# Kernel tuning notes

Measured on AMD Instinct MI355X. Metric: run time of the kernel, lower is better.

The kernel has to match this reference:

```python
import jax, jax.numpy as jnp
import numpy as np

B, T, E, H, VIN, VOUT = 64, 64, 64, 128, 256, 32000


def setup_inputs() -> dict:
    key = jax.random.key(0)
    ks = jax.random.split(key, 14)
    s = 0.08  # ~1/sqrt(hidden), torch-style init scale, avoids gate saturation
    return {
        "src": jax.random.randint(ks[0], (B, T), 0, VIN),
        "tgt": jax.random.randint(ks[1], (B, T), 0, VOUT),
        "enc_emb": jax.random.normal(ks[2], (VIN, E), jnp.float32) * s,
        "dec_emb": jax.random.normal(ks[3], (VOUT, E), jnp.float32) * s,
        "enc_Wih": jax.random.normal(ks[4], (4 * H, E), jnp.float32) * s,
        "enc_Whh": jax.random.normal(ks[5], (4 * H, H), jnp.float32) * s,
        "enc_bih": jax.random.normal(ks[6], (4 * H,), jnp.float32) * s,
        "enc_bhh": jax.random.normal(ks[7], (4 * H,), jnp.float32) * s,
        "dec_Wih": jax.random.normal(ks[8], (4 * H, E), jnp.float32) * s,
        "dec_Whh": jax.random.normal(ks[9], (4 * H, H), jnp.float32) * s,
        "dec_bih": jax.random.normal(ks[10], (4 * H,), jnp.float32) * s,
        "dec_bhh": jax.random.normal(ks[11], (4 * H,), jnp.float32) * s,
        "fc_W": jax.random.normal(ks[12], (VOUT, H), jnp.float32) * s,
        "fc_b": jax.random.normal(ks[13], (VOUT,), jnp.float32) * s,
    }


def _lstm(xs, h0, c0, Wih, Whh, bih, bhh):
    # xs: [T, B, E]; torch gate order i, f, g, o
    xg = jnp.einsum('tbe,ge->tbg', xs, Wih) + bih  # precompute input gates for all steps

    def step(carry, xg_t):
        h, c = carry
        gates = xg_t + h @ Whh.T + bhh  # [B, 4H]
        i, f, g, o = jnp.split(gates, 4, axis=-1)
        c = jax.nn.sigmoid(f) * c + jax.nn.sigmoid(i) * jnp.tanh(g)
        h = jax.nn.sigmoid(o) * jnp.tanh(c)
        return (h, c), h

    (h, c), hs = jax.lax.scan(step, (h0, c0), xg)
    return h, c, hs


def reference(src, tgt, enc_emb, dec_emb, enc_Wih, enc_Whh, enc_bih, enc_bhh,
              dec_Wih, dec_Whh, dec_bih, dec_bhh, fc_W, fc_b):
    # padding_idx=0: row 0 of embeddings is zero
    enc_emb = enc_emb.at[0].set(0.0)
    dec_emb = dec_emb.at[0].set(0.0)

    zeros = jnp.zeros((src.shape[0], H), jnp.float32)
    # encoder over full src
    x_src = enc_emb[src].transpose(1, 0, 2)  # [T, B, E]
    h, c, _ = _lstm(x_src, zeros, zeros, enc_Wih, enc_Whh, enc_bih, enc_bhh)
    # decoder with full teacher forcing: inputs are tgt[:, :-1]
    x_dec = dec_emb[tgt[:, :-1]].transpose(1, 0, 2)  # [T-1, B, E]
    _, _, hs = _lstm(x_dec, h, c, dec_Wih, dec_Whh, dec_bih, dec_bhh)
    logits = jnp.einsum('tbh,vh->tbv', hs, fc_W) + fc_b  # [T-1, B, V]
    out = jnp.concatenate(
        [jnp.zeros((1,) + logits.shape[1:], logits.dtype), logits], axis=0)
    return out.transpose(1, 0, 2)  # [B, T, V]; outputs[:, 0] == 0 as in torch
```

## Files before the change

kernel.cpp:

```cpp
#include <hip/hip_runtime.h>
#include <hip/hip_bf16.h>
#include <stddef.h>

#define BB 64
#define TTOT 64
#define EE 64
#define HH 128
#define G4 512
#define VIN 256
#define VOUT 32000

typedef __attribute__((ext_vector_type(8))) short bf16x8;
typedef __attribute__((ext_vector_type(4))) float f32x4;

__device__ __forceinline__ unsigned short f2bf(float x) {
    unsigned int u = __float_as_uint(x);
    unsigned int r = (u + 0x7fffu + ((u >> 16) & 1u)) >> 16;
    return (unsigned short)r;
}

__device__ __forceinline__ float fsig(float x) {
    return 1.f / (1.f + __expf(-x));
}
__device__ __forceinline__ float ftanh(float x) {
    return 1.f - 2.f / (__expf(2.f * x) + 1.f);
}

__device__ __forceinline__ float quad_sum(float v) {
    v += __int_as_float(__builtin_amdgcn_mov_dpp(__float_as_int(v), 0xB1, 0xF, 0xF, true));
    v += __int_as_float(__builtin_amdgcn_mov_dpp(__float_as_int(v), 0x4E, 0xF, 0xF, true));
    return v;
}

__device__ __forceinline__ int hidx(int u) { return u + (u >> 5) * 8; }
#define HPAD 152

__global__ void conv_bf16(const float* __restrict__ in, unsigned short* __restrict__ out, int n4) {
    int i = blockIdx.x * blockDim.x + threadIdx.x;
    if (i < n4) {
        float4 v = *(const float4*)(in + i * 4);
        ushort4 o;
        o.x = f2bf(v.x); o.y = f2bf(v.y); o.z = f2bf(v.z); o.w = f2bf(v.w);
        *(ushort4*)(out + i * 4) = o;
    }
}

__global__ __launch_bounds__(512) void enc_table_k(const float* __restrict__ emb,
                                                   const float* __restrict__ Wih,
                                                   const float* __restrict__ bih,
                                                   float* __restrict__ table) {
    int v = blockIdx.x;
    int g = threadIdx.x;
    __shared__ __align__(16) float x[EE];
    if (g < EE) x[g] = (v == 0) ? 0.f : emb[(size_t)v * EE + g];
    __syncthreads();
    float acc = bih[g];
    const float* wr = Wih + (size_t)g * EE;
#pragma unroll
    for (int e = 0; e < EE; e += 4) {
        float4 w4 = *(const float4*)(wr + e);
        float4 x4 = *(const float4*)(&x[e]);
        acc = fmaf(x4.x, w4.x, acc);
        acc = fmaf(x4.y, w4.y, acc);
        acc = fmaf(x4.z, w4.z, acc);
        acc = fmaf(x4.w, w4.w, acc);
    }
    table[(size_t)v * G4 + g] = acc;
}

__global__ __launch_bounds__(512) void xg_dec_k(const int* __restrict__ tgt,
                                                const float* __restrict__ emb,
                                                const float* __restrict__ Wih,
                                                const float* __restrict__ bih,
                                                float* __restrict__ xg) {
    int p0 = blockIdx.x * 8;
    int g = threadIdx.x;
    __shared__ __align__(16) float x[8][EE];
    {
        int pr = g >> 6, e = g & 63;
        int pair = p0 + pr;
        int t = pair >> 6, b = pair & 63;
        int tok = tgt[b * TTOT + t];
        x[pr][e] = (tok == 0) ? 0.f : emb[(size_t)tok * EE + e];
    }
    __syncthreads();
    float bi = bih[g];
    float acc[8];
#pragma unroll
    for (int pr = 0; pr < 8; ++pr) acc[pr] = bi;
    const float* wr = Wih + (size_t)g * EE;
#pragma unroll
    for (int e = 0; e < EE; e += 4) {
        float4 w4 = *(const float4*)(wr + e);
#pragma unroll
        for (int pr = 0; pr < 8; ++pr) {
            float4 x4 = *(const float4*)(&x[pr][e]);
            acc[pr] = fmaf(x4.x, w4.x, acc[pr]);
            acc[pr] = fmaf(x4.y, w4.y, acc[pr]);
            acc[pr] = fmaf(x4.z, w4.z, acc[pr]);
            acc[pr] = fmaf(x4.w, w4.w, acc[pr]);
        }
    }
#pragma unroll
    for (int pr = 0; pr < 8; ++pr)
        xg[(size_t)(p0 + pr) * G4 + g] = acc[pr];
}

__global__ __launch_bounds__(512) void lstm_k(const float* __restrict__ table,
                                              const int* __restrict__ src,
                                              const float* __restrict__ eWhh,
                                              const float* __restrict__ ebhh,
                                              const float* __restrict__ xg,
                                              const float* __restrict__ dWhh,
                                              const float* __restrict__ dbhh,
                                              unsigned short* __restrict__ hs) {
    int b = blockIdx.x;
    int tid = threadIdx.x;
    int u = tid >> 2, p = tid & 3;
    __shared__ __align__(16) float hbuf[2][HPAD];
    __shared__ int toks[TTOT];

    float w[4][32];
#pragma unroll
    for (int q = 0; q < 4; ++q) {
        const float* wr = eWhh + (size_t)(q * HH + u) * HH + p * 32;
#pragma unroll
        for (int kk = 0; kk < 32; kk += 4) {
            float4 t4 = *(const float4*)(wr + kk);
            w[q][kk] = t4.x; w[q][kk + 1] = t4.y; w[q][kk + 2] = t4.z; w[q][kk + 3] = t4.w;
        }
    }
    if (tid < TTOT) toks[tid] = src[b * TTOT + tid];
    if (p == 0) {
        hbuf[0][hidx(u)] = 0.f;
        hs[((size_t)b << 13) + u] = 0;
    }
    float bb = ebhh[p * HH + u];
    float c = 0.f;
    __syncthreads();

    float xv = table[(size_t)toks[0] * G4 + p * HH + u];

#pragma unroll 1
    for (int t = 0; t < TTOT; ++t) {
        float xn = (t + 1 < TTOT) ? table[(size_t)toks[t + 1] * G4 + p * HH + u] : 0.f;
        const float* hq = &hbuf[t & 1][p * 40];
        float4 h4[8];
#pragma unroll
        for (int j = 0; j < 8; ++j) h4[j] = *(const float4*)(hq + j * 4);

        float v0 = (p == 0) ? (xv + bb) : 0.f;
        float v1 = (p == 1) ? (xv + bb) : 0.f;
        float v2 = (p == 2) ? (xv + bb) : 0.f;
        float v3 = (p == 3) ? (xv + bb) : 0.f;
#pragma unroll
        for (int j = 0; j < 8; ++j) {
            float4 h = h4[j];
#define FMA4(hc, kk)                              \
            v0 = fmaf(hc, w[0][kk], v0);          \
            v1 = fmaf(hc, w[1][kk], v1);          \
            v2 = fmaf(hc, w[2][kk], v2);          \
            v3 = fmaf(hc, w[3][kk], v3);
            FMA4(h.x, j * 4 + 0) FMA4(h.y, j * 4 + 1) FMA4(h.z, j * 4 + 2) FMA4(h.w, j * 4 + 3)
#undef FMA4
        }
        v0 = quad_sum(v0); v1 = quad_sum(v1); v2 = quad_sum(v2); v3 = quad_sum(v3);

        float fi = fsig(v0), ff = fsig(v1), fg = ftanh(v2), fo = fsig(v3);
        c = ff * c + fi * fg;
        float hn = fo * ftanh(c);
        if (p == 0) hbuf[(t + 1) & 1][hidx(u)] = hn;
        __syncthreads();
        xv = xn;
    }

#pragma unroll
    for (int q = 0; q < 4; ++q) {
        const float* wr = dWhh + (size_t)(q * HH + u) * HH + p * 32;
#pragma unroll
        for (int kk = 0; kk < 32; kk += 4) {
            float4 t4 = *(const float4*)(wr + kk);
            w[q][kk] = t4.x; w[q][kk + 1] = t4.y; w[q][kk + 2] = t4.z; w[q][kk + 3] = t4.w;
        }
    }
    bb = dbhh[p * HH + u];
    float xv2 = xg[(size_t)b * G4 + p * HH + u];

#pragma unroll 1
    for (int t = 0; t < TTOT - 1; ++t) {
        float xn = (t + 1 < TTOT - 1) ? xg[((size_t)(t + 1) * BB + b) * G4 + p * HH + u] : 0.f;
        const float* hq = &hbuf[t & 1][p * 40];
        float4 h4[8];
#pragma unroll
        for (int j = 0; j < 8; ++j) h4[j] = *(const float4*)(hq + j * 4);

        float v0 = (p == 0) ? (xv2 + bb) : 0.f;
        float v1 = (p == 1) ? (xv2 + bb) : 0.f;
        float v2 = (p == 2) ? (xv2 + bb) : 0.f;
        float v3 = (p == 3) ? (xv2 + bb) : 0.f;
#pragma unroll
        for (int j = 0; j < 8; ++j) {
            float4 h = h4[j];
#define FMA4(hc, kk)                              \
            v0 = fmaf(hc, w[0][kk], v0);          \
            v1 = fmaf(hc, w[1][kk], v1);          \
            v2 = fmaf(hc, w[2][kk], v2);          \
            v3 = fmaf(hc, w[3][kk], v3);
            FMA4(h.x, j * 4 + 0) FMA4(h.y, j * 4 + 1) FMA4(h.z, j * 4 + 2) FMA4(h.w, j * 4 + 3)
#undef FMA4
        }
        v0 = quad_sum(v0); v1 = quad_sum(v1); v2 = quad_sum(v2); v3 = quad_sum(v3);

        float fi = fsig(v0), ff = fsig(v1), fg = ftanh(v2), fo = fsig(v3);
        c = ff * c + fi * fg;
        float hn = fo * ftanh(c);
        if (p == 0) {
            hbuf[(t + 1) & 1][hidx(u)] = hn;
            hs[((size_t)b << 13) + ((size_t)(t + 1) << 7) + u] = f2bf(hn);
        }
        __syncthreads();
        xv2 = xn;
    }
}

#define LDSW 260
__global__ __launch_bounds__(256) void fc_k(const unsigned short* __restrict__ hs,
                                            const unsigned short* __restrict__ fw,
                                            const float* __restrict__ fb,
                                            float* __restrict__ out) {
    int id = blockIdx.x;
    int bq = id / 125;
    int nb = id % 125;
    int n0 = nb * 256;
    int wave = threadIdx.x >> 6;
    int lane = threadIdx.x & 63;
    int l15 = lane & 15;
    int kg = lane >> 4;

    __shared__ __align__(16) float lds[64 * LDSW];

    bf16x8 a[4][4];
#pragma unroll
    for (int i = 0; i < 4; ++i) {
        const unsigned short* arow = fw + (size_t)(n0 + (wave * 4 + i) * 16 + l15) * HH + kg * 8;
#pragma unroll
        for (int kt = 0; kt < 4; ++kt) a[i][kt] = *(const bf16x8*)(arow + kt * 32);
    }

    float4 biasv = *(const float4*)(fb + n0 + lane * 4);

#pragma unroll 1
    for (int bi = 0; bi < 16; ++bi) {
        int b = bq * 16 + bi;

        const unsigned short* ph = hs + ((size_t)b << 13);
        bf16x8 bfr[4][4];
#pragma unroll
        for (int ts = 0; ts < 4; ++ts) {
            const unsigned short* pr = ph + ((size_t)(ts * 16 + l15) << 7) + kg * 8;
#pragma unroll
            for (int kt = 0; kt < 4; ++kt) bfr[ts][kt] = *(const bf16x8*)(pr + kt * 32);
        }

#pragma unroll
        for (int i = 0; i < 4; ++i) {
            f32x4 ac0 = (f32x4){0.f, 0.f, 0.f, 0.f};
            f32x4 ac1 = (f32x4){0.f, 0.f, 0.f, 0.f};
            f32x4 ac2 = (f32x4){0.f, 0.f, 0.f, 0.f};
            f32x4 ac3 = (f32x4){0.f, 0.f, 0.f, 0.f};
#pragma unroll
            for (int kt = 0; kt < 4; ++kt) {
                ac0 = __builtin_amdgcn_mfma_f32_16x16x32_bf16(a[i][kt], bfr[0][kt], ac0, 0, 0, 0);
                ac1 = __builtin_amdgcn_mfma_f32_16x16x32_bf16(a[i][kt], bfr[1][kt], ac1, 0, 0, 0);
                ac2 = __builtin_amdgcn_mfma_f32_16x16x32_bf16(a[i][kt], bfr[2][kt], ac2, 0, 0, 0);
                ac3 = __builtin_amdgcn_mfma_f32_16x16x32_bf16(a[i][kt], bfr[3][kt], ac3, 0, 0, 0);
            }
            int nc = (wave * 4 + i) * 16 + kg * 4;
#define DUMP(ts, accv)                                                         \
            *(f32x4*)(&lds[(ts * 16 + l15) * LDSW + nc]) = accv;
            DUMP(0, ac0) DUMP(1, ac1) DUMP(2, ac2) DUMP(3, ac3)
#undef DUMP
        }
        __syncthreads();

        size_t outb = (size_t)b * TTOT * VOUT + n0 + lane * 4;
#pragma unroll
        for (int r = 0; r < 16; ++r) {
            int ot = wave * 16 + r;
            f32x4 v;
            if (ot == 0) {
                v = (f32x4){0.f, 0.f, 0.f, 0.f};
            } else {
                f32x4 s = *(const f32x4*)(&lds[ot * LDSW + lane * 4]);
                v[0] = s[0] + biasv.x; v[1] = s[1] + biasv.y;
                v[2] = s[2] + biasv.z; v[3] = s[3] + biasv.w;
            }
            __builtin_nontemporal_store(v, (f32x4*)(out + outb + (size_t)ot * VOUT));
        }
        __syncthreads();
    }
}

extern "C" void kernel_launch(void* const* d_in, const int* in_sizes, int n_in,
                              void* d_out, int out_size, void* d_ws, size_t ws_size,
                              hipStream_t stream) {
    const int* src = (const int*)d_in[0];
    const int* tgt = (const int*)d_in[1];
    const float* enc_emb = (const float*)d_in[2];
    const float* dec_emb = (const float*)d_in[3];
    const float* enc_Wih = (const float*)d_in[4];
    const float* enc_Whh = (const float*)d_in[5];
    const float* enc_bih = (const float*)d_in[6];
    const float* enc_bhh = (const float*)d_in[7];
    const float* dec_Wih = (const float*)d_in[8];
    const float* dec_Whh = (const float*)d_in[9];
    const float* dec_bih = (const float*)d_in[10];
    const float* dec_bhh = (const float*)d_in[11];
    const float* fc_W = (const float*)d_in[12];
    const float* fc_b = (const float*)d_in[13];
    float* out = (float*)d_out;
    char* ws = (char*)d_ws;

    float* table = (float*)(ws + 0);
    unsigned short* hs = (unsigned short*)(ws + 524288);
    unsigned short* fwb = (unsigned short*)(ws + 1572864);
    float* xgd = (float*)(ws + 9764864);

    enc_table_k<<<VIN, 512, 0, stream>>>(enc_emb, enc_Wih, enc_bih, table);
    xg_dec_k<<<(63 * 64) / 8, 512, 0, stream>>>(tgt, dec_emb, dec_Wih, dec_bih, xgd);
    conv_bf16<<<(VOUT * HH / 4 + 255) / 256, 256, 0, stream>>>(fc_W, fwb, VOUT * HH / 4);
    lstm_k<<<BB, 512, 0, stream>>>(table, src, enc_Whh, enc_bhh, xgd, dec_Whh, dec_bhh, hs);
    fc_k<<<4 * 125, 256, 0, stream>>>(hs, fwb, fc_b, out);
}
```

Baseline: 267.1 us.

## Merge prep kernels, overlap fc weight conversion with LSTM, use packed FMA

Merges the encoder table and decoder input-gate kernels into one launch, with 16 pairs per decoder block. The fc_W bf16 conversion moves into extra blocks of the LSTM kernel so it runs on otherwise idle CUs during the serial recurrence. The recurrent matvec switches to v_pk_fma_f32 on float pairs to halve FMA instruction count on the latency-bound critical path. This removes two launches and hides the conversion, at the cost of inline asm, a changed summation order, and extra blocks competing with the 64 LSTM blocks.

```diff
diff --git a/kernel.cpp b/kernel.cpp
--- a/kernel.cpp
+++ b/kernel.cpp
@@ -12,6 +12,7 @@
 
 typedef __attribute__((ext_vector_type(8))) short bf16x8;
 typedef __attribute__((ext_vector_type(4))) float f32x4;
+typedef __attribute__((ext_vector_type(2))) float f32x2;
 
 __device__ __forceinline__ unsigned short f2bf(float x) {
     unsigned int u = __float_as_uint(x);
@@ -26,6 +27,11 @@
     return 1.f - 2.f / (__expf(2.f * x) + 1.f);
 }
 
+__device__ __forceinline__ f32x2 pkfma(f32x2 a, f32x2 b, f32x2 d) {
+    asm("v_pk_fma_f32 %0, %1, %2, %0" : "+v"(d) : "v"(a), "v"(b));
+    return d;
+}
+
 __device__ __forceinline__ float quad_sum(float v) {
     v += __int_as_float(__builtin_amdgcn_mov_dpp(__float_as_int(v), 0xB1, 0xF, 0xF, true));
     v += __int_as_float(__builtin_amdgcn_mov_dpp(__float_as_int(v), 0x4E, 0xF, 0xF, true));
@@ -35,75 +41,68 @@
 __device__ __forceinline__ int hidx(int u) { return u + (u >> 5) * 8; }
 #define HPAD 152
 
-__global__ void conv_bf16(const float* __restrict__ in, unsigned short* __restrict__ out, int n4) {
-    int i = blockIdx.x * blockDim.x + threadIdx.x;
-    if (i < n4) {
-        float4 v = *(const float4*)(in + i * 4);
-        ushort4 o;
-        o.x = f2bf(v.x); o.y = f2bf(v.y); o.z = f2bf(v.z); o.w = f2bf(v.w);
-        *(ushort4*)(out + i * 4) = o;
-    }
-}
-
-__global__ __launch_bounds__(512) void enc_table_k(const float* __restrict__ emb,
-                                                   const float* __restrict__ Wih,
-                                                   const float* __restrict__ bih,
-                                                   float* __restrict__ table) {
-    int v = blockIdx.x;
+__global__ __launch_bounds__(512) void prep_k(const float* __restrict__ enc_emb,
+                                              const float* __restrict__ eWih,
+                                              const float* __restrict__ ebih,
+                                              float* __restrict__ table,
+                                              const int* __restrict__ tgt,
+                                              const float* __restrict__ dec_emb,
+                                              const float* __restrict__ dWih,
+                                              const float* __restrict__ dbih,
+                                              float* __restrict__ xg) {
+    __shared__ __align__(16) float x[16][EE];
     int g = threadIdx.x;
-    __shared__ __align__(16) float x[EE];
-    if (g < EE) x[g] = (v == 0) ? 0.f : emb[(size_t)v * EE + g];
-    __syncthreads();
-    float acc = bih[g];
-    const float* wr = Wih + (size_t)g * EE;
-#pragma unroll
-    for (int e = 0; e < EE; e += 4) {
-        float4 w4 = *(const float4*)(wr + e);
-        float4 x4 = *(const float4*)(&x[e]);
-        acc = fmaf(x4.x, w4.x, acc);
-        acc = fmaf(x4.y, w4.y, acc);
-        acc = fmaf(x4.z, w4.z, acc);
-        acc = fmaf(x4.w, w4.w, acc);
-    }
-    table[(size_t)v * G4 + g] = acc;
-}
-
-__global__ __launch_bounds__(512) void xg_dec_k(const int* __restrict__ tgt,
-                                                const float* __restrict__ emb,
-                                                const float* __restrict__ Wih,
-                                                const float* __restrict__ bih,
-                                                float* __restrict__ xg) {
-    int p0 = blockIdx.x * 8;
-    int g = threadIdx.x;
-    __shared__ __align__(16) float x[8][EE];
-    {
-        int pr = g >> 6, e = g & 63;
-        int pair = p0 + pr;
-        int t = pair >> 6, b = pair & 63;
-        int tok = tgt[b * TTOT + t];
-        x[pr][e] = (tok == 0) ? 0.f : emb[(size_t)tok * EE + e];
-    }
-    __syncthreads();
-    float bi = bih[g];
-    float acc[8];
-#pragma unroll
-    for (int pr = 0; pr < 8; ++pr) acc[pr] = bi;
-    const float* wr = Wih + (size_t)g * EE;
-#pragma unroll
-    for (int e = 0; e < EE; e += 4) {
-        float4 w4 = *(const float4*)(wr + e);
-#pragma unroll
-        for (int pr = 0; pr < 8; ++pr) {
-            float4 x4 = *(const float4*)(&x[pr][e]);
-            acc[pr] = fmaf(x4.x, w4.x, acc[pr]);
-            acc[pr] = fmaf(x4.y, w4.y, acc[pr]);
-            acc[pr] = fmaf(x4.z, w4.z, acc[pr]);
-            acc[pr] = fmaf(x4.w, w4.w, acc[pr]);
-        }
-    }
-#pragma unroll
-    for (int pr = 0; pr < 8; ++pr)
-        xg[(size_t)(p0 + pr) * G4 + g] = acc[pr];
+    if (blockIdx.x < 256) {
+        int v = blockIdx.x;
+        if (g < EE) x[0][g] = (v == 0) ? 0.f : enc_emb[(size_t)v * EE + g];
+        __syncthreads();
+        float acc = ebih[g];
+        const float* wr = eWih + (size_t)g * EE;
+#pragma unroll
+        for (int e = 0; e < EE; e += 4) {
+            float4 w4 = *(const float4*)(wr + e);
+            float4 x4 = *(const float4*)(&x[0][e]);
+            acc = fmaf(x4.x, w4.x, acc);
+            acc = fmaf(x4.y, w4.y, acc);
+            acc = fmaf(x4.z, w4.z, acc);
+            acc = fmaf(x4.w, w4.w, acc);
+        }
+        table[(size_t)v * G4 + g] = acc;
+    } else {
+        int p0 = (blockIdx.x - 256) * 16;
+        {
+            int e = g & 63;
+#pragma unroll
+            for (int half = 0; half < 2; ++half) {
+                int pr = (g >> 6) + half * 8;
+                int pair = p0 + pr;
+                int t = pair >> 6, b = pair & 63;
+                int tok = tgt[b * TTOT + t];
+                x[pr][e] = (tok == 0) ? 0.f : dec_emb[(size_t)tok * EE + e];
+            }
+        }
+        __syncthreads();
+        float bi = dbih[g];
+        float acc[16];
+#pragma unroll
+        for (int pr = 0; pr < 16; ++pr) acc[pr] = bi;
+        const float* wr = dWih + (size_t)g * EE;
+#pragma unroll
+        for (int e = 0; e < EE; e += 4) {
+            float4 w4 = *(const float4*)(wr + e);
+#pragma unroll
+            for (int pr = 0; pr < 16; ++pr) {
+                float4 x4 = *(const float4*)(&x[pr][e]);
+                acc[pr] = fmaf(x4.x, w4.x, acc[pr]);
+                acc[pr] = fmaf(x4.y, w4.y, acc[pr]);
+                acc[pr] = fmaf(x4.z, w4.z, acc[pr]);
+                acc[pr] = fmaf(x4.w, w4.w, acc[pr]);
+            }
+        }
+#pragma unroll
+        for (int pr = 0; pr < 16; ++pr)
+            xg[(size_t)(p0 + pr) * G4 + g] = acc[pr];
+    }
 }
 
 __global__ __launch_bounds__(512) void lstm_k(const float* __restrict__ table,
@@ -113,21 +112,38 @@
                                               const float* __restrict__ xg,
                                               const float* __restrict__ dWhh,
                                               const float* __restrict__ dbhh,
-                                              unsigned short* __restrict__ hs) {
+                                              unsigned short* __restrict__ hs,
+                                              const float* __restrict__ fcW,
+                                              unsigned short* __restrict__ fwb) {
+    if (blockIdx.x >= BB) {
+        int i0 = (blockIdx.x - BB) * 512 + threadIdx.x;
+        const int n4 = VOUT * HH / 4;
+        const int stride = 512 * 512;
+#pragma unroll 1
+        for (int i = i0; i < n4; i += stride) {
+            float4 v = *(const float4*)(fcW + (size_t)i * 4);
+            ushort4 o;
+            o.x = f2bf(v.x); o.y = f2bf(v.y); o.z = f2bf(v.z); o.w = f2bf(v.w);
+            *(ushort4*)(fwb + (size_t)i * 4) = o;
+        }
+        return;
+    }
+
     int b = blockIdx.x;
     int tid = threadIdx.x;
     int u = tid >> 2, p = tid & 3;
     __shared__ __align__(16) float hbuf[2][HPAD];
     __shared__ int toks[TTOT];
 
-    float w[4][32];
+    f32x2 w2[4][16];
 #pragma unroll
     for (int q = 0; q < 4; ++q) {
         const float* wr = eWhh + (size_t)(q * HH + u) * HH + p * 32;
 #pragma unroll
         for (int kk = 0; kk < 32; kk += 4) {
             float4 t4 = *(const float4*)(wr + kk);
-            w[q][kk] = t4.x; w[q][kk + 1] = t4.y; w[q][kk + 2] = t4.z; w[q][kk + 3] = t4.w;
+            w2[q][kk >> 1] = (f32x2){t4.x, t4.y};
+            w2[q][(kk >> 1) + 1] = (f32x2){t4.z, t4.w};
         }
     }
     if (tid < TTOT) toks[tid] = src[b * TTOT + tid];
@@ -149,21 +165,22 @@
 #pragma unroll
         for (int j = 0; j < 8; ++j) h4[j] = *(const float4*)(hq + j * 4);
 
-        float v0 = (p == 0) ? (xv + bb) : 0.f;
-        float v1 = (p == 1) ? (xv + bb) : 0.f;
-        float v2 = (p == 2) ? (xv + bb) : 0.f;
-        float v3 = (p == 3) ? (xv + bb) : 0.f;
+        f32x2 a0 = (f32x2){0.f, 0.f}, a1 = a0, a2 = a0, a3 = a0;
 #pragma unroll
         for (int j = 0; j < 8; ++j) {
             float4 h = h4[j];
-#define FMA4(hc, kk)                              \
-            v0 = fmaf(hc, w[0][kk], v0);          \
-            v1 = fmaf(hc, w[1][kk], v1);          \
-            v2 = fmaf(hc, w[2][kk], v2);          \
-            v3 = fmaf(hc, w[3][kk], v3);
-            FMA4(h.x, j * 4 + 0) FMA4(h.y, j * 4 + 1) FMA4(h.z, j * 4 + 2) FMA4(h.w, j * 4 + 3)
-#undef FMA4
-        }
+            f32x2 hlo = (f32x2){h.x, h.y};
+            f32x2 hhi = (f32x2){h.z, h.w};
+            a0 = pkfma(hlo, w2[0][2 * j], a0); a0 = pkfma(hhi, w2[0][2 * j + 1], a0);
+            a1 = pkfma(hlo, w2[1][2 * j], a1); a1 = pkfma(hhi, w2[1][2 * j + 1], a1);
+            a2 = pkfma(hlo, w2[2][2 * j], a2); a2 = pkfma(hhi, w2[2][2 * j + 1], a2);
+            a3 = pkfma(hlo, w2[3][2 * j], a3); a3 = pkfma(hhi, w2[3][2 * j + 1], a3);
+        }
+        float xb = xv + bb;
+        float v0 = a0[0] + a0[1] + (p == 0 ? xb : 0.f);
+        float v1 = a1[0] + a1[1] + (p == 1 ? xb : 0.f);
+        float v2 = a2[0] + a2[1] + (p == 2 ? xb : 0.f);
+        float v3 = a3[0] + a3[1] + (p == 3 ? xb : 0.f);
         v0 = quad_sum(v0); v1 = quad_sum(v1); v2 = quad_sum(v2); v3 = quad_sum(v3);
 
         float fi = fsig(v0), ff = fsig(v1), fg = ftanh(v2), fo = fsig(v3);
@@ -180,7 +197,8 @@
 #pragma unroll
         for (int kk = 0; kk < 32; kk += 4) {
             float4 t4 = *(const float4*)(wr + kk);
-            w[q][kk] = t4.x; w[q][kk + 1] = t4.y; w[q][kk + 2] = t4.z; w[q][kk + 3] = t4.w;
+            w2[q][kk >> 1] = (f32x2){t4.x, t4.y};
+            w2[q][(kk >> 1) + 1] = (f32x2){t4.z, t4.w};
         }
     }
     bb = dbhh[p * HH + u];
@@ -194,21 +212,22 @@
 #pragma unroll
         for (int j = 0; j < 8; ++j) h4[j] = *(const float4*)(hq + j * 4);
 
-        float v0 = (p == 0) ? (xv2 + bb) : 0.f;
-        float v1 = (p == 1) ? (xv2 + bb) : 0.f;
-        float v2 = (p == 2) ? (xv2 + bb) : 0.f;
-        float v3 = (p == 3) ? (xv2 + bb) : 0.f;
+        f32x2 a0 = (f32x2){0.f, 0.f}, a1 = a0, a2 = a0, a3 = a0;
 #pragma unroll
         for (int j = 0; j < 8; ++j) {
             float4 h = h4[j];
-#define FMA4(hc, kk)                              \
-            v0 = fmaf(hc, w[0][kk], v0);          \
-            v1 = fmaf(hc, w[1][kk], v1);          \
-            v2 = fmaf(hc, w[2][kk], v2);          \
-            v3 = fmaf(hc, w[3][kk], v3);
-            FMA4(h.x, j * 4 + 0) FMA4(h.y, j * 4 + 1) FMA4(h.z, j * 4 + 2) FMA4(h.w, j * 4 + 3)
-#undef FMA4
-        }
+            f32x2 hlo = (f32x2){h.x, h.y};
+            f32x2 hhi = (f32x2){h.z, h.w};
+            a0 = pkfma(hlo, w2[0][2 * j], a0); a0 = pkfma(hhi, w2[0][2 * j + 1], a0);
+            a1 = pkfma(hlo, w2[1][2 * j], a1); a1 = pkfma(hhi, w2[1][2 * j + 1], a1);
+            a2 = pkfma(hlo, w2[2][2 * j], a2); a2 = pkfma(hhi, w2[2][2 * j + 1], a2);
+            a3 = pkfma(hlo, w2[3][2 * j], a3); a3 = pkfma(hhi, w2[3][2 * j + 1], a3);
+        }
+        float xb = xv2 + bb;
+        float v0 = a0[0] + a0[1] + (p == 0 ? xb : 0.f);
+        float v1 = a1[0] + a1[1] + (p == 1 ? xb : 0.f);
+        float v2 = a2[0] + a2[1] + (p == 2 ? xb : 0.f);
+        float v3 = a3[0] + a3[1] + (p == 3 ? xb : 0.f);
         v0 = quad_sum(v0); v1 = quad_sum(v1); v2 = quad_sum(v2); v3 = quad_sum(v3);
 
         float fi = fsig(v0), ff = fsig(v1), fg = ftanh(v2), fo = fsig(v3);
@@ -326,9 +345,9 @@
     unsigned short* fwb = (unsigned short*)(ws + 1572864);
     float* xgd = (float*)(ws + 9764864);
 
-    enc_table_k<<<VIN, 512, 0, stream>>>(enc_emb, enc_Wih, enc_bih, table);
-    xg_dec_k<<<(63 * 64) / 8, 512, 0, stream>>>(tgt, dec_emb, dec_Wih, dec_bih, xgd);
-    conv_bf16<<<(VOUT * HH / 4 + 255) / 256, 256, 0, stream>>>(fc_W, fwb, VOUT * HH / 4);
-    lstm_k<<<BB, 512, 0, stream>>>(table, src, enc_Whh, enc_bhh, xgd, dec_Whh, dec_bhh, hs);
+    prep_k<<<256 + 252, 512, 0, stream>>>(enc_emb, enc_Wih, enc_bih, table,
+                                          tgt, dec_emb, dec_Wih, dec_bih, xgd);
+    lstm_k<<<BB + 512, 512, 0, stream>>>(table, src, enc_Whh, enc_bhh, xgd,
+                                         dec_Whh, dec_bhh, hs, fc_W, fwb);
     fc_k<<<4 * 125, 256, 0, stream>>>(hs, fwb, fc_b, out);
 }
```

After: 247.7 us. -7.3%, faster.
